# Performance work log

Hardware: AMD Instinct MI355X
Metric: run time of the kernel (lower is better)

## Reference

```python
import jax, jax.numpy as jnp
import numpy as np

B, T, E, H = 1024, 200, 128, 128
N_ITEMS, N_CATS = 100000, 1000
LN_EPS = 1e-5


def _prelu(x, a):
    return jnp.where(x >= 0, x, a * x)


def _layernorm(x, g, b):
    m = x.mean(-1, keepdims=True)
    v = ((x - m) ** 2).mean(-1, keepdims=True)
    return (x - m) / jnp.sqrt(v + LN_EPS) * g + b


def setup_inputs() -> dict:
    key = jax.random.key(0)
    it = iter(jax.random.split(key, 64))
    nx = lambda: next(it)
    def lin(out_d, in_d):
        s = 1.0 / np.sqrt(in_d)
        return jax.random.uniform(nx(), (out_d, in_d), jnp.float32, -s, s)
    inp = {}
    inp['behavior_ids'] = jax.random.randint(nx(), (B, T), 0, N_ITEMS)
    inp['candidate_id'] = jax.random.randint(nx(), (B,), 0, N_ITEMS)
    inp['candidate_cat'] = jax.random.randint(nx(), (B,), 0, N_CATS)
    inp['dense_features'] = jax.random.normal(nx(), (B, 5), jnp.float32)
    inp['item_emb'] = (jax.random.normal(nx(), (N_ITEMS, E), jnp.float32) * 0.01).at[0].set(0.0)
    inp['cat_emb'] = (jax.random.normal(nx(), (N_CATS, E // 2), jnp.float32) * 0.01).at[0].set(0.0)
    # nn.GRU params (gate order r,z,n)
    inp['gru_wih'] = lin(3 * H, E)
    inp['gru_whh'] = lin(3 * H, H)
    inp['gru_bih'] = jnp.zeros((3 * H,), jnp.float32)
    inp['gru_bhh'] = jnp.zeros((3 * H,), jnp.float32)
    # auxiliary_net: Linear(H,E) -> ReLU -> Linear(E,1)
    inp['aux_w1'] = lin(E, H); inp['aux_b1'] = jnp.zeros((E,), jnp.float32)
    inp['aux_w2'] = lin(1, E); inp['aux_b2'] = jnp.zeros((1,), jnp.float32)
    # attention_mlp: Linear(3H,64) -> PReLU -> Linear(64,1)
    inp['att_w1'] = lin(64, 3 * H); inp['att_b1'] = jnp.zeros((64,), jnp.float32)
    inp['att_a'] = jnp.array(0.25, jnp.float32)
    inp['att_w2'] = lin(1, 64); inp['att_b2'] = jnp.zeros((1,), jnp.float32)
    # AUGRU gates: Linear(2H, H) each
    inp['wz'] = lin(H, 2 * H); inp['bz'] = jnp.zeros((H,), jnp.float32)
    inp['wr'] = lin(H, 2 * H); inp['br'] = jnp.zeros((H,), jnp.float32)
    inp['wh'] = lin(H, 2 * H); inp['bh'] = jnp.zeros((H,), jnp.float32)
    # dense_proj Linear(5,32)
    inp['dp_w'] = lin(32, 5); inp['dp_b'] = jnp.zeros((32,), jnp.float32)
    # MLP: 352 -> 256 -> 128 -> 64, each Linear + LayerNorm + PReLU
    dims = [H + E + E // 2 + 32, 256, 128, 64]
    for i in range(3):
        inp[f'm_w{i+1}'] = lin(dims[i + 1], dims[i])
        inp[f'm_b{i+1}'] = jnp.zeros((dims[i + 1],), jnp.float32)
        inp[f'ln_g{i+1}'] = jnp.ones((dims[i + 1],), jnp.float32)
        inp[f'ln_b{i+1}'] = jnp.zeros((dims[i + 1],), jnp.float32)
        inp[f'pa{i+1}'] = jnp.array(0.25, jnp.float32)
    # 3 task heads Linear(64,1), stacked
    inp['heads_w'] = lin(3, 64); inp['heads_b'] = jnp.zeros((3,), jnp.float32)
    return inp


def _forward_core(behavior_ids, candidate_id, candidate_cat, dense_features,
                  item_emb, cat_emb, gru_wih, gru_whh, gru_bih, gru_bhh,
                  aux_w1, aux_b1, aux_w2, aux_b2,
                  att_w1, att_b1, att_a, att_w2, att_b2,
                  wz, bz, wr, br, wh, bh, dp_w, dp_b,
                  m_w1, m_b1, ln_g1, ln_b1, pa1,
                  m_w2, m_b2, ln_g2, ln_b2, pa2,
                  m_w3, m_b3, ln_g3, ln_b3, pa3,
                  heads_w, heads_b):
    beh = item_emb[behavior_ids]            # [B,T,E]
    cand = item_emb[candidate_id]           # [B,E]
    catv = cat_emb[candidate_cat]           # [B,E//2]
    Bsz = beh.shape[0]
    Hd = gru_whh.shape[1]
    h0 = jnp.zeros((Bsz, Hd), beh.dtype)
    # --- interest extractor GRU (cuDNN GRU math, gate order r,z,n) ---
    xp = jnp.einsum('bte,ge->btg', beh, gru_wih) + gru_bih  # [B,T,3H]
    def gru_step(h, x):
        hp = h @ gru_whh.T + gru_bhh
        xr, xz, xn = jnp.split(x, 3, -1)
        hr, hz, hn = jnp.split(hp, 3, -1)
        r = jax.nn.sigmoid(xr + hr)
        z = jax.nn.sigmoid(xz + hz)
        n = jnp.tanh(xn + r * hn)
        hnew = (1 - z) * n + z * h
        return hnew, hnew
    _, hs = jax.lax.scan(gru_step, h0, jnp.swapaxes(xp, 0, 1))
    hs = jnp.swapaxes(hs, 0, 1)             # [B,T,H]
    # --- auxiliary logits ---
    aux = jax.nn.relu(hs[:, :-1] @ aux_w1.T + aux_b1) @ aux_w2.T + aux_b2  # [B,T-1,1]
    # --- attention (embed_dim == hidden_size so cand_proj == candidate_emb) ---
    ce = cand[:, None, :]
    att_in = jnp.concatenate([hs, jnp.broadcast_to(ce, hs.shape), hs * ce], -1)  # [B,T,3H]
    scores = (_prelu(att_in @ att_w1.T + att_b1, att_a) @ att_w2.T + att_b2)[..., 0]
    att = jax.nn.softmax(scores, axis=-1)   # [B,T]
    # --- AUGRU: attention-modulated update gate ---
    def augru_step(h, xs):
        x, a = xs                           # x: [B,H], a: [B]
        comb = jnp.concatenate([x, h], -1)
        z = jax.nn.sigmoid(comb @ wz.T + bz)
        r = jax.nn.sigmoid(comb @ wr.T + br)
        comb_r = jnp.concatenate([x, r * h], -1)
        ht = jnp.tanh(comb_r @ wh.T + bh)
        zp = a[:, None] * z
        return (1 - zp) * h + zp * ht, None
    hT, _ = jax.lax.scan(augru_step, h0, (jnp.swapaxes(hs, 0, 1), att.T))
    # --- fusion MLP (dropout is identity in eval) ---
    dense_out = dense_features @ dp_w.T + dp_b
    x = jnp.concatenate([hT, cand, catv, dense_out], -1)  # [B,352]
    for (w, b, g, be, a) in ((m_w1, m_b1, ln_g1, ln_b1, pa1),
                             (m_w2, m_b2, ln_g2, ln_b2, pa2),
                             (m_w3, m_b3, ln_g3, ln_b3, pa3)):
        x = _prelu(_layernorm(x @ w.T + b, g, be), a)
    preds = jax.nn.sigmoid(x @ heads_w.T + heads_b)  # [B,3] == 3 heads of [B,1]
    return preds, aux


def reference(behavior_ids, candidate_id, candidate_cat, dense_features,
              item_emb, cat_emb, gru_wih, gru_whh, gru_bih, gru_bhh,
              aux_w1, aux_b1, aux_w2, aux_b2,
              att_w1, att_b1, att_a, att_w2, att_b2,
              wz, bz, wr, br, wh, bh, dp_w, dp_b,
              m_w1, m_b1, ln_g1, ln_b1, pa1,
              m_w2, m_b2, ln_g2, ln_b2, pa2,
              m_w3, m_b3, ln_g3, ln_b3, pa3,
              heads_w, heads_b):
    return _forward_core(behavior_ids, candidate_id, candidate_cat, dense_features,
                         item_emb, cat_emb, gru_wih, gru_whh, gru_bih, gru_bhh,
                         aux_w1, aux_b1, aux_w2, aux_b2,
                         att_w1, att_b1, att_a, att_w2, att_b2,
                         wz, bz, wr, br, wh, bh, dp_w, dp_b,
                         m_w1, m_b1, ln_g1, ln_b1, pa1,
                         m_w2, m_b2, ln_g2, ln_b2, pa2,
                         m_w3, m_b3, ln_g3, ln_b3, pa3,
                         heads_w, heads_b)
```

## Files before the change

### kernel.cpp

```cpp
#include <hip/hip_runtime.h>


typedef __bf16 bf16;
typedef float f32x4 __attribute__((ext_vector_type(4)));
typedef __bf16 bf16x8 __attribute__((ext_vector_type(8)));
typedef __bf16 bf16x4 __attribute__((ext_vector_type(4)));

#define MFMA16(a, b, c) __builtin_amdgcn_mfma_f32_16x16x32_bf16((a), (b), (c), 0, 0, 0)

#define BATCH 1024
#define SEQT 200
#define F32_ONE 0x3F800000u

__device__ __forceinline__ float sigm(float x) {
  return __builtin_amdgcn_rcpf(1.0f + __expf(-x));
}
__device__ __forceinline__ float tanh_fast(float x) {
  float ax = fabsf(x);
  float t = 1.0f - 2.0f * __builtin_amdgcn_rcpf(__expf(2.0f * ax) + 1.0f);
  return copysignf(t, x);
}

__device__ __forceinline__ void bar_lgkm() {
  asm volatile("s_waitcnt lgkmcnt(0)\n\ts_barrier" ::: "memory");
// ... 34 lines not shown
}

template <typename DT>
__device__ __forceinline__ void prep_body(
    const int* __restrict__ cid, const int* __restrict__ ccat,
    const DT* __restrict__ dense, const DT* __restrict__ item_emb,
    const DT* __restrict__ cat_emb, const DT* __restrict__ dp_w,
    const DT* __restrict__ dp_b, bf16* __restrict__ candbuf, bf16* __restrict__ xf) {
  const int b = blockIdx.x;
  const int t = threadIdx.x;
  bf16 v = (bf16)ldf(item_emb, (long)cid[b] * 128 + t);
  candbuf[b * 128 + t] = v;
  xf[(long)b * 352 + 128 + t] = v;
  if (t < 64) xf[(long)b * 352 + 256 + t] = (bf16)ldf(cat_emb, (long)ccat[b] * 64 + t);
  if (t < 32) {
    float s = ldf(dp_b, t);
    for (int k = 0; k < 5; k++) s += ldf(dense, b * 5 + k) * ldf(dp_w, t * 5 + k);
    xf[(long)b * 352 + 320 + t] = (bf16)s;
  }
}
__global__ __launch_bounds__(128) void k_prep(
    const unsigned* __restrict__ disc, const int* cid, const int* ccat,
    const void* dense, const void* item_emb, const void* cat_emb,
    const void* dp_w, const void* dp_b, bf16* candbuf, bf16* xf) {
  if (*disc == F32_ONE)
    prep_body<float>(cid, ccat, (const float*)dense, (const float*)item_emb,
                     (const float*)cat_emb, (const float*)dp_w, (const float*)dp_b, candbuf, xf);
  else
    prep_body<bf16>(cid, ccat, (const bf16*)dense, (const bf16*)item_emb,
                    (const bf16*)cat_emb, (const bf16*)dp_w, (const bf16*)dp_b, candbuf, xf);
}

template <typename DT>
__device__ __forceinline__ void gru5_body(
    const int* __restrict__ ids, const bf16* __restrict__ ieb,
    const DT* __restrict__ wih, const DT* __restrict__ whh,
    const DT* __restrict__ bih, const DT* __restrict__ bhh, bf16* __restrict__ hs,
    bf16 (*hA)[16][136], bf16 (*xb)[4][16][128]) {
  const int b0 = blockIdx.x * 16;
  const int tid = threadIdx.x;
  const int w = tid >> 6, lane = tid & 63, l15 = lane & 15, quad = lane >> 4;
  const int nc = w * 16 + l15;

  for (int i = tid; i < 2 * 16 * 136; i += 512) ((bf16*)hA)[i] = (bf16)0.0f;

  bf16x8 wir[4], wiz[4], win_[4], whr[4], whz[4], whn[4];
#pragma unroll
  for (int k = 0; k < 4; k++) {
    const long off = k * 32 + quad * 8;
    wir[k] = ld8(wih, (long)nc * 128 + off);
    wiz[k] = ld8(wih, (long)(128 + nc) * 128 + off);
    win_[k] = ld8(wih, (long)(256 + nc) * 128 + off);
    whr[k] = ld8(whh, (long)nc * 128 + off);
    whz[k] = ld8(whh, (long)(128 + nc) * 128 + off);
    whn[k] = ld8(whh, (long)(256 + nc) * 128 + off);
  }
  const float br_s = ldf(bih, nc) + ldf(bhh, nc);
  const float bz_s = ldf(bih, 128 + nc) + ldf(bhh, 128 + nc);
  const float bxn_s = ldf(bih, 256 + nc);
  const float bhn_s = ldf(bhh, 256 + nc);

  const int idrow = (tid >> 4) & 15;
  const int* idbase = ids + (long)(b0 + idrow) * SEQT;
  const int srcoff = ((tid & 15) ^ (idrow & 7)) * 8;

  auto DMA = [&](const int4 id4, int buf) {
#pragma unroll
    for (int j = 0; j < 2; j++) {
      const int slot = j * 2 + (tid >> 8);
      dma16(ieb + (long)((&id4.x)[slot]) * 128 + srcoff,
            (char*)&xb[buf][0][0][0] + (j * 512 + tid) * 16);
    }
  };

  const int srow = tid >> 5, sch = (tid & 31) * 4;
  bf16* hsb = hs + ((long)(b0 + srow) * SEQT) * 128 + sch;

  float hreg[4] = {0.f, 0.f, 0.f, 0.f};
  const f32x4 z4 = {0.f, 0.f, 0.f, 0.f};

  int4 idv = *(const int4*)(idbase);
  DMA(idv, 0);
  idv = *(const int4*)(idbase + 4);
  asm volatile("s_waitcnt vmcnt(1)" ::: "memory");
  __builtin_amdgcn_sched_barrier(0);
  __builtin_amdgcn_s_barrier();

#define GRU_STEP(P, S, WAITC)                                                  \
  {                                                                            \
    const int tt = t0 + (S);                                                   \
    bf16x8 af[4], xaf[4];                                                      \
    _Pragma("unroll") for (int k = 0; k < 4; k++) {                            \
      af[k] = *(const bf16x8*)&hA[P][l15][k * 32 + quad * 8];                  \
      xaf[k] = *(const bf16x8*)((const char*)&xb[buf][S][0][0] + l15 * 256 +   \
                                ((((k << 2) + quad) ^ (l15 & 7)) << 4));       \
    }                                                                          \
    { const int slot = tt ? tt - 1 : 0;                                        \
      bf16x4 hv = *(const bf16x4*)&hA[P][srow][sch];                           \
      *(bf16x4*)(hsb + (long)slot * 128) = hv; }                               \
    f32x4 ar = z4, az = z4, axn = z4, ahn = z4;                                \
    _Pragma("unroll") for (int k = 0; k < 4; k++) {                            \
      ar = MFMA16(xaf[k], wir[k], ar);                                         \
      az = MFMA16(xaf[k], wiz[k], az);                                         \
      axn = MFMA16(xaf[k], win_[k], axn);                                      \
    }                                                                          \
    _Pragma("unroll") for (int k = 0; k < 4; k++) {                            \
      ar = MFMA16(af[k], whr[k], ar);                                          \
      az = MFMA16(af[k], whz[k], az);                                          \
      ahn = MFMA16(af[k], whn[k], ahn);                                        \
    }                                                                          \
    _Pragma("unroll") for (int r = 0; r < 4; r++) {                            \
      float r_ = sigm(ar[r] + br_s);                                           \
      float z_ = sigm(az[r] + bz_s);                                           \
      float n_ = tanh_fast(axn[r] + bxn_s + r_ * (ahn[r] + bhn_s));            \
      float hnew = (1.0f - z_) * n_ + z_ * hreg[r];                            \
      hreg[r] = hnew;                                                          \
      hA[(P) ^ 1][quad * 4 + r][nc] = (bf16)hnew;                              \
    }                                                                          \
    if (WAITC) {                                                               \
       \
      asm volatile("s_waitcnt vmcnt(5) lgkmcnt(0)\n\ts_barrier" ::: "memory"); \
    } else {                                                                   \
      bar_lgkm();                                                              \
    }                                                                          \
  }

  for (int c = 0; c < 50; c++) {
    const int t0 = c * 4;
    const int buf = c & 1;
    if (c < 49) {
      DMA(idv, buf ^ 1);
      int nid = (c + 2) * 4; if (nid > 196) nid = 196;
      idv = *(const int4*)(idbase + nid);
    }
    GRU_STEP(0, 0, 0) GRU_STEP(1, 1, 0) GRU_STEP(0, 2, 0) GRU_STEP(1, 3, (c < 49))
  }
#undef GRU_STEP
  { bf16x4 hv = *(const bf16x4*)&hA[0][srow][sch];
    *(bf16x4*)(hsb + (long)(SEQT - 1) * 128) = hv; }
}
__global__ __launch_bounds__(512, 1) void k_gru5(
    const unsigned* __restrict__ disc, const int* ids, const bf16* ieb,
    const void* wih, const void* whh, const void* bih, const void* bhh, bf16* hs) {
  __shared__ __align__(16) bf16 hA[2][16][136];
  __shared__ __align__(16) bf16 xb[2][4][16][128];
  if (*disc == F32_ONE)
    gru5_body<float>(ids, ieb, (const float*)wih, (const float*)whh,
                     (const float*)bih, (const float*)bhh, hs, hA, xb);
  else
    gru5_body<bf16>(ids, ieb, (const bf16*)wih, (const bf16*)whh,
                    (const bf16*)bih, (const bf16*)bhh, hs, hA, xb);
}

template <typename DT>
__device__ __forceinline__ void attaux_body(
    const bf16* __restrict__ hs, const int* __restrict__ cid,
    const DT* __restrict__ item_emb,
    const DT* __restrict__ aw1, const DT* __restrict__ ab1,
    const DT* __restrict__ aw2, const DT* __restrict__ ab2,
    const DT* __restrict__ tw1, const DT* __restrict__ tb1, const DT* __restrict__ ta,
    const DT* __restrict__ tw2, const DT* __restrict__ tb2,
    float* __restrict__ sc, float* __restrict__ outaux,
    bf16 (*As)[64][128], float (*scPt)[64], float (*scPa)[64]) {
  const int t0 = blockIdx.x * 64;
  const int b0 = blockIdx.y * 16;
  const int tid = threadIdx.x, w = tid >> 6, lane = tid & 63, l15 = lane & 15, quad = lane >> 4;

  const int tn = w * 16 + l15;
  bf16x8 wth[4], wtc[4], wthc[4], wa0[4], wa1[4];
#pragma unroll
  for (int k = 0; k < 4; k++) {
    const long off = k * 32 + quad * 8;
    wth[k]  = ld8(tw1, (long)tn * 384 + off);
    wtc[k]  = ld8(tw1, (long)tn * 384 + 128 + off);
    wthc[k] = ld8(tw1, (long)tn * 384 + 256 + off);
    wa0[k]  = ld8(aw1, (long)((2 * w) * 16 + l15) * 128 + off);
    wa1[k]  = ld8(aw1, (long)((2 * w + 1) * 16 + l15) * 128 + off);
  }
  const float tb1c = ldf(tb1, tn), tw2c = ldf(tw2, tn);
  const float ab1c0 = ldf(ab1, (2 * w) * 16 + l15), aw2c0 = ldf(aw2, (2 * w) * 16 + l15);
  const float ab1c1 = ldf(ab1, (2 * w + 1) * 16 + l15), aw2c1 = ldf(aw2, (2 * w + 1) * 16 + l15);
  const float aP = ldf(ta, 0), tb2s = ldf(tb2, 0), ab2s = ldf(ab2, 0);

// ... 95 lines not shown
    const void* aw1, const void* ab1, const void* aw2, const void* ab2,
    const void* tw1, const void* tb1, const void* ta, const void* tw2, const void* tb2,
    float* sc, float* outaux) {
  __shared__ __align__(16) bf16 As[2][64][128];
  __shared__ __align__(16) float scPt[4][64];
  __shared__ __align__(16) float scPa[4][64];
  if (*disc == F32_ONE)
    attaux_body<float>(hs, cid, (const float*)item_emb,
                       (const float*)aw1, (const float*)ab1, (const float*)aw2, (const float*)ab2,
                       (const float*)tw1, (const float*)tb1, (const float*)ta,
                       (const float*)tw2, (const float*)tb2, sc, outaux, As, scPt, scPa);
  else
    attaux_body<bf16>(hs, cid, (const bf16*)item_emb,
                      (const bf16*)aw1, (const bf16*)ab1, (const bf16*)aw2, (const bf16*)ab2,
                      (const bf16*)tw1, (const bf16*)tb1, (const bf16*)ta,
                      (const bf16*)tw2, (const bf16*)tb2, sc, outaux, As, scPt, scPa);
}

__global__ __launch_bounds__(256) void k_softmax(float* __restrict__ sc) {
  const int b = blockIdx.x, tid = threadIdx.x;
  __shared__ float red[256];
  float v = (tid < SEQT) ? sc[(long)b * SEQT + tid] : -1e30f;
  red[tid] = v; __syncthreads();
  for (int s = 128; s > 0; s >>= 1) { if (tid < s) red[tid] = fmaxf(red[tid], red[tid + s]); __syncthreads(); }
  float mx = red[0]; __syncthreads();
  float e = (tid < SEQT) ? __expf(v - mx) : 0.f;
  red[tid] = e; __syncthreads();
  for (int s = 128; s > 0; s >>= 1) { if (tid < s) red[tid] += red[tid + s]; __syncthreads(); }
  float inv = 1.0f / red[0];
  if (tid < SEQT) sc[(long)b * SEQT + tid] = e * inv;
}

template <typename DT>
__device__ __forceinline__ void augru5_body(
    const bf16* __restrict__ hsrc, const float* __restrict__ att,
    const DT* __restrict__ wz, const DT* __restrict__ wr, const DT* __restrict__ wh,
    const DT* __restrict__ bzv, const DT* __restrict__ brv, const DT* __restrict__ bhv,
    bf16* __restrict__ xf_out,
    bf16 (*hA)[16][136], bf16 (*rhA)[136], float (*attL)[201],
    bf16 (*xb)[4][16][128]) {
  const int b0 = blockIdx.x * 16;
  const int tid = threadIdx.x;
  const int w = tid >> 6, lane = tid & 63, l15 = lane & 15, quad = lane >> 4;
  const int nc = w * 16 + l15;

  for (int i = tid; i < 2 * 16 * 136; i += 512) ((bf16*)hA)[i] = (bf16)0.0f;
  for (int i = tid; i < 16 * SEQT; i += 512) {
    int r = i / SEQT, c = i - r * SEQT;
    attL[r][c] = att[(long)(b0 + r) * SEQT + c];
  }

  bf16x8 wzx[4], wzh[4], wrx[4], wrh[4], whx[4], whh_[4];
#pragma unroll
  for (int k = 0; k < 4; k++) {
    const long off = k * 32 + quad * 8;
    wzx[k] = ld8(wz, (long)nc * 256 + off);
    wzh[k] = ld8(wz, (long)nc * 256 + 128 + off);
    wrx[k] = ld8(wr, (long)nc * 256 + off);
    wrh[k] = ld8(wr, (long)nc * 256 + 128 + off);
    whx[k] = ld8(wh, (long)nc * 256 + off);
    whh_[k] = ld8(wh, (long)nc * 256 + 128 + off);
  }
  const float bz_s = ldf(bzv, nc);
  const float br_s = ldf(brv, nc);
  const float bh_s = ldf(bhv, nc);

  const int drow = (tid >> 4) & 15;
  const int srcoff = ((tid & 15) ^ (drow & 7)) * 8;
  auto DMA = [&](int t0, int buf) {
#pragma unroll
    for (int j = 0; j < 2; j++) {
      const int slot = j * 2 + (tid >> 8);
      dma16(hsrc + ((long)(b0 + drow) * SEQT + t0 + slot) * 128 + srcoff,
            (char*)&xb[buf][0][0][0] + (j * 512 + tid) * 16);
    }
  };

  float hreg[4] = {0.f, 0.f, 0.f, 0.f};
  const f32x4 z4 = {0.f, 0.f, 0.f, 0.f};

  DMA(0, 0);
  asm volatile("s_waitcnt vmcnt(0)" ::: "memory");
  __builtin_amdgcn_sched_barrier(0);
  __builtin_amdgcn_s_barrier();

#define AUGRU_STEP(P, S, WAITC)                                                \
  {                                                                            \
    const int tt = t0 + (S);                                                   \
    bf16x8 af[4], xaf[4];                                                      \
    _Pragma("unroll") for (int k = 0; k < 4; k++) {                            \
      af[k] = *(const bf16x8*)&hA[P][l15][k * 32 + quad * 8];                  \
      xaf[k] = *(const bf16x8*)((const char*)&xb[buf][S][0][0] + l15 * 256 +   \
                                ((((k << 2) + quad) ^ (l15 & 7)) << 4));       \
    }                                                                          \
    f32x4 az = z4, ar = z4, axh = z4;                                          \
    _Pragma("unroll") for (int k = 0; k < 4; k++) {                            \
      az = MFMA16(xaf[k], wzx[k], az);                                         \
      ar = MFMA16(xaf[k], wrx[k], ar);                                         \
      axh = MFMA16(xaf[k], whx[k], axh);                                       \
    }                                                                          \
    _Pragma("unroll") for (int k = 0; k < 4; k++) {                            \
      az = MFMA16(af[k], wzh[k], az);                                          \
      ar = MFMA16(af[k], wrh[k], ar);                                          \
    }                                                                          \
    float zp[4];                                                               \
    _Pragma("unroll") for (int r = 0; r < 4; r++) {                            \
      float a_ = attL[quad * 4 + r][tt];                                       \
      float z_ = sigm(az[r] + bz_s);                                           \
      float r_ = sigm(ar[r] + br_s);                                           \
      zp[r] = a_ * z_;                                                         \
      rhA[quad * 4 + r][nc] = (bf16)(r_ * hreg[r]);                            \
    }                                                                          \
    bar_lgkm();                                                                \
    bf16x8 rf[4];                                                              \
    _Pragma("unroll") for (int k = 0; k < 4; k++)                              \
      rf[k] = *(const bf16x8*)&rhA[l15][k * 32 + quad * 8];                    \
    f32x4 ahh = axh;                                                           \
    _Pragma("unroll") for (int k = 0; k < 4; k++)                              \
      ahh = MFMA16(rf[k], whh_[k], ahh);                                       \
    _Pragma("unroll") for (int r = 0; r < 4; r++) {                            \
      float ht = tanh_fast(ahh[r] + bh_s);                                     \
      float hnew = (1.f - zp[r]) * hreg[r] + zp[r] * ht;                       \
      hreg[r] = hnew;                                                          \
      hA[(P) ^ 1][quad * 4 + r][nc] = (bf16)hnew;                              \
    }                                                                          \
    if (WAITC) {                                                               \
                     \
      asm volatile("s_waitcnt vmcnt(0) lgkmcnt(0)\n\ts_barrier" ::: "memory"); \
    } else {                                                                   \
      bar_lgkm();                                                              \
    }                                                                          \
  }

  for (int c = 0; c < 50; c++) {
    const int t0 = c * 4;
    const int buf = c & 1;
    if (c < 49) DMA((c + 1) * 4, buf ^ 1);
    AUGRU_STEP(0, 0, 0) AUGRU_STEP(1, 1, 0) AUGRU_STEP(0, 2, 0) AUGRU_STEP(1, 3, (c < 49))
  }
#undef AUGRU_STEP
#pragma unroll
  for (int r = 0; r < 4; r++)
    xf_out[(long)(b0 + quad * 4 + r) * 352 + nc] = (bf16)hreg[r];
}
__global__ __launch_bounds__(512, 1) void k_augru5(
    const unsigned* __restrict__ disc, const bf16* hsrc, const float* att,
    const void* wz, const void* wr, const void* wh,
    const void* bzv, const void* brv, const void* bhv, bf16* xf_out) {
  __shared__ __align__(16) bf16 hA[2][16][136];
  __shared__ __align__(16) bf16 rhA[16][136];
  __shared__ __align__(16) float attL[16][201];
  __shared__ __align__(16) bf16 xb[2][4][16][128];
  if (*disc == F32_ONE)
    augru5_body<float>(hsrc, att, (const float*)wz, (const float*)wr, (const float*)wh,
                       (const float*)bzv, (const float*)brv, (const float*)bhv, xf_out,
                       hA, rhA, attL, xb);
  else
    augru5_body<bf16>(hsrc, att, (const bf16*)wz, (const bf16*)wr, (const bf16*)wh,
                      (const bf16*)bzv, (const bf16*)brv, (const bf16*)bhv, xf_out,
                      hA, rhA, attL, xb);
}

template <typename DT>
__device__ __forceinline__ void mlp_body(
    const bf16* __restrict__ xf,
    const DT* __restrict__ w1, const DT* __restrict__ b1, const DT* __restrict__ g1, const DT* __restrict__ be1, const DT* __restrict__ pa1,
    const DT* __restrict__ w2, const DT* __restrict__ b2, const DT* __restrict__ g2, const DT* __restrict__ be2, const DT* __restrict__ pa2,
    const DT* __restrict__ w3, const DT* __restrict__ b3, const DT* __restrict__ g3, const DT* __restrict__ be3, const DT* __restrict__ pa3,
    const DT* __restrict__ hw, const DT* __restrict__ hb, float* __restrict__ preds,
    float (*xs)[352], float (*ys)[256]) {
  const int tid = threadIdx.x, w = tid >> 6, lane = tid & 63;
  const int b = blockIdx.x * 4 + w;
  for (int i = lane; i < 352; i += 64) xs[w][i] = (float)xf[(long)b * 352 + i];
  __syncthreads();
  float acc1[4];
#pragma unroll
  for (int oi = 0; oi < 4; oi++) {
    int o = lane + 64 * oi;
    float s = ldf(b1, o);
    for (int k = 0; k < 352; k += 8) {
      bf16x8 wv = ld8(w1, (long)o * 352 + k);
#pragma unroll
      for (int j = 0; j < 8; j++) s += xs[w][k + j] * (float)wv[j];
    }
    acc1[oi] = s;
  }
  float sm = acc1[0] + acc1[1] + acc1[2] + acc1[3];
#pragma unroll
  for (int m = 1; m < 64; m <<= 1) sm += __shfl_xor(sm, m, 64);
  float mean = sm * (1.0f / 256.0f);
  float vs = 0.f;
// ... 121 lines not shown
  const void* dp_b = d_in[26];
  const void* m_w1 = d_in[27];
  const void* m_b1 = d_in[28];
  const void* ln_g1 = d_in[29];
  const void* ln_b1 = d_in[30];
  const void* pa1 = d_in[31];
  const void* m_w2 = d_in[32];
  const void* m_b2 = d_in[33];
  const void* ln_g2 = d_in[34];
  const void* ln_b2 = d_in[35];
  const void* pa2 = d_in[36];
  const void* m_w3 = d_in[37];
  const void* m_b3 = d_in[38];
  const void* ln_g3 = d_in[39];
  const void* ln_b3 = d_in[40];
  const void* pa3 = d_in[41];
  const void* heads_w = d_in[42];
  const void* heads_b = d_in[43];
  (void)in_sizes; (void)n_in; (void)out_size; (void)ws_size;

  const unsigned* disc = (const unsigned*)ln_g1;

  char* ws = (char*)d_ws;
  bf16* HS = (bf16*)(ws);
  float* SC = (float*)(ws + 52428800L);
  bf16* CAND = (bf16*)(ws + 53248000L);
  bf16* XF = (bf16*)(ws + 53510144L);
  bf16* IEB = (bf16*)(ws + 54231040L);
  float* OUT = (float*)d_out;

  k_cast<<<6250, 256, 0, stream>>>(disc, item_emb, IEB);
  k_prep<<<BATCH, 128, 0, stream>>>(disc, candidate_id, candidate_cat, dense, item_emb,
                                    cat_emb, dp_w, dp_b, CAND, XF);
  k_gru5<<<64, 512, 0, stream>>>(disc, behavior_ids, IEB, gru_wih, gru_whh,
                                 gru_bih, gru_bhh, HS);
  k_attaux<<<dim3(4, 64), 256, 0, stream>>>(disc, HS, candidate_id, item_emb,
                                            aux_w1, aux_b1, aux_w2, aux_b2,
                                            att_w1, att_b1, att_a, att_w2, att_b2,
                                            SC, OUT + 3072);
  k_softmax<<<BATCH, 256, 0, stream>>>(SC);
  k_augru5<<<64, 512, 0, stream>>>(disc, HS, SC, wz, wr, wh, bz, br, bh, XF);
  k_mlp<<<256, 256, 0, stream>>>(disc, XF,
      m_w1, m_b1, ln_g1, ln_b1, pa1,
      m_w2, m_b2, ln_g2, ln_b2, pa2,
      m_w3, m_b3, ln_g3, ln_b3, pa3,
      heads_w, heads_b, OUT);
}
```

Before: 733.9 us.

## Halve GRU/AUGRU block to 4 waves, each computing two 16-column tiles

Both recurrent kernels now launch 256 threads (4 waves) per block instead of 512, and each wave handles 32 hidden columns as two 16-wide MFMA tiles. Weight fragments are doubled per wave, the DMA and hidden-state store loops are widened to cover the same data with fewer threads. The aim is cheaper per-step barriers and more independent MFMAs per wave to hide latency in the sequential loop. In exchange, register pressure roughly doubles and each wave does twice the serial gate math per step.

```diff
diff --git a/kernel.cpp b/kernel.cpp
--- a/kernel.cpp
+++ b/kernel.cpp
@@ -90,7 +90,7 @@
 }
 
 template <typename DT>
-__device__ __forceinline__ void gru5_body(
+__device__ __forceinline__ void gru6_body(
     const int* __restrict__ ids, const bf16* __restrict__ ieb,
     const DT* __restrict__ wih, const DT* __restrict__ whh,
     const DT* __restrict__ bih, const DT* __restrict__ bhh, bf16* __restrict__ hs,
@@ -98,43 +98,45 @@
   const int b0 = blockIdx.x * 16;
   const int tid = threadIdx.x;
   const int w = tid >> 6, lane = tid & 63, l15 = lane & 15, quad = lane >> 4;
-  const int nc = w * 16 + l15;
-
-  for (int i = tid; i < 2 * 16 * 136; i += 512) ((bf16*)hA)[i] = (bf16)0.0f;
-
-  bf16x8 wir[4], wiz[4], win_[4], whr[4], whz[4], whn[4];
-#pragma unroll
-  for (int k = 0; k < 4; k++) {
-    const long off = k * 32 + quad * 8;
-    wir[k] = ld8(wih, (long)nc * 128 + off);
-    wiz[k] = ld8(wih, (long)(128 + nc) * 128 + off);
-    win_[k] = ld8(wih, (long)(256 + nc) * 128 + off);
-    whr[k] = ld8(whh, (long)nc * 128 + off);
-    whz[k] = ld8(whh, (long)(128 + nc) * 128 + off);
-    whn[k] = ld8(whh, (long)(256 + nc) * 128 + off);
-  }
-  const float br_s = ldf(bih, nc) + ldf(bhh, nc);
-  const float bz_s = ldf(bih, 128 + nc) + ldf(bhh, 128 + nc);
-  const float bxn_s = ldf(bih, 256 + nc);
-  const float bhn_s = ldf(bhh, 256 + nc);
-
-  const int idrow = (tid >> 4) & 15;
-  const int* idbase = ids + (long)(b0 + idrow) * SEQT;
-  const int srcoff = ((tid & 15) ^ (idrow & 7)) * 8;
+
+  for (int i = tid; i < 2 * 16 * 136; i += 256) ((bf16*)hA)[i] = (bf16)0.0f;
+
+  bf16x8 wir[2][4], wiz[2][4], win_[2][4], whr[2][4], whz[2][4], whn[2][4];
+  float br_s[2], bz_s[2], bxn_s[2], bhn_s[2];
+#pragma unroll
+  for (int nt = 0; nt < 2; nt++) {
+    const int nc = w * 32 + nt * 16 + l15;
+#pragma unroll
+    for (int k = 0; k < 4; k++) {
+      const long off = k * 32 + quad * 8;
+      wir[nt][k] = ld8(wih, (long)nc * 128 + off);
+      wiz[nt][k] = ld8(wih, (long)(128 + nc) * 128 + off);
+      win_[nt][k] = ld8(wih, (long)(256 + nc) * 128 + off);
+      whr[nt][k] = ld8(whh, (long)nc * 128 + off);
+      whz[nt][k] = ld8(whh, (long)(128 + nc) * 128 + off);
+      whn[nt][k] = ld8(whh, (long)(256 + nc) * 128 + off);
+    }
+    br_s[nt] = ldf(bih, nc) + ldf(bhh, nc);
+    bz_s[nt] = ldf(bih, 128 + nc) + ldf(bhh, 128 + nc);
+    bxn_s[nt] = ldf(bih, 256 + nc);
+    bhn_s[nt] = ldf(bhh, 256 + nc);
+  }
+
+  const int drow = tid >> 4;
+  const int* idbase = ids + (long)(b0 + drow) * SEQT;
+  const int srcoff = ((tid & 15) ^ (drow & 7)) * 8;
 
   auto DMA = [&](const int4 id4, int buf) {
 #pragma unroll
-    for (int j = 0; j < 2; j++) {
-      const int slot = j * 2 + (tid >> 8);
-      dma16(ieb + (long)((&id4.x)[slot]) * 128 + srcoff,
-            (char*)&xb[buf][0][0][0] + (j * 512 + tid) * 16);
-    }
+    for (int j = 0; j < 4; j++)
+      dma16(ieb + (long)((&id4.x)[j]) * 128 + srcoff,
+            (char*)&xb[buf][0][0][0] + (j * 256 + tid) * 16);
   };
 
-  const int srow = tid >> 5, sch = (tid & 31) * 4;
+  const int srow = tid >> 4, sch = (tid & 15) * 8;
   bf16* hsb = hs + ((long)(b0 + srow) * SEQT) * 128 + sch;
 
-  float hreg[4] = {0.f, 0.f, 0.f, 0.f};
+  float hreg[2][4] = {{0.f, 0.f, 0.f, 0.f}, {0.f, 0.f, 0.f, 0.f}};
   const f32x4 z4 = {0.f, 0.f, 0.f, 0.f};
 
   int4 idv = *(const int4*)(idbase);
@@ -154,26 +156,33 @@
                                 ((((k << 2) + quad) ^ (l15 & 7)) << 4));       \
     }                                                                          \
     { const int slot = tt ? tt - 1 : 0;                                        \
-      bf16x4 hv = *(const bf16x4*)&hA[P][srow][sch];                           \
-      *(bf16x4*)(hsb + (long)slot * 128) = hv; }                               \
-    f32x4 ar = z4, az = z4, axn = z4, ahn = z4;                                \
-    _Pragma("unroll") for (int k = 0; k < 4; k++) {                            \
-      ar = MFMA16(xaf[k], wir[k], ar);                                         \
-      az = MFMA16(xaf[k], wiz[k], az);                                         \
-      axn = MFMA16(xaf[k], win_[k], axn);                                      \
-    }                                                                          \
-    _Pragma("unroll") for (int k = 0; k < 4; k++) {                            \
-      ar = MFMA16(af[k], whr[k], ar);                                          \
-      az = MFMA16(af[k], whz[k], az);                                          \
-      ahn = MFMA16(af[k], whn[k], ahn);                                        \
-    }                                                                          \
-    _Pragma("unroll") for (int r = 0; r < 4; r++) {                            \
-      float r_ = sigm(ar[r] + br_s);                                           \
-      float z_ = sigm(az[r] + bz_s);                                           \
-      float n_ = tanh_fast(axn[r] + bxn_s + r_ * (ahn[r] + bhn_s));            \
-      float hnew = (1.0f - z_) * n_ + z_ * hreg[r];                            \
-      hreg[r] = hnew;                                                          \
-      hA[(P) ^ 1][quad * 4 + r][nc] = (bf16)hnew;                              \
+      bf16x8 hv = *(const bf16x8*)&hA[P][srow][sch];                           \
+      *(bf16x8*)(hsb + (long)slot * 128) = hv; }                               \
+    f32x4 ar[2] = {z4, z4}, az[2] = {z4, z4}, axn[2] = {z4, z4},               \
+          ahn[2] = {z4, z4};                                                   \
+    _Pragma("unroll") for (int k = 0; k < 4; k++)                              \
+    _Pragma("unroll") for (int nt = 0; nt < 2; nt++) {                         \
+      ar[nt] = MFMA16(xaf[k], wir[nt][k], ar[nt]);                             \
+      az[nt] = MFMA16(xaf[k], wiz[nt][k], az[nt]);                             \
+      axn[nt] = MFMA16(xaf[k], win_[nt][k], axn[nt]);                          \
+    }                                                                          \
+    _Pragma("unroll") for (int k = 0; k < 4; k++)                              \
+    _Pragma("unroll") for (int nt = 0; nt < 2; nt++) {                         \
+      ar[nt] = MFMA16(af[k], whr[nt][k], ar[nt]);                              \
+      az[nt] = MFMA16(af[k], whz[nt][k], az[nt]);                              \
+      ahn[nt] = MFMA16(af[k], whn[nt][k], ahn[nt]);                            \
+    }                                                                          \
+    _Pragma("unroll") for (int nt = 0; nt < 2; nt++) {                         \
+      const int nc = w * 32 + nt * 16 + l15;                                   \
+      _Pragma("unroll") for (int r = 0; r < 4; r++) {                          \
+        float r_ = sigm(ar[nt][r] + br_s[nt]);                                 \
+        float z_ = sigm(az[nt][r] + bz_s[nt]);                                 \
+        float n_ = tanh_fast(axn[nt][r] + bxn_s[nt] +                          \
+                             r_ * (ahn[nt][r] + bhn_s[nt]));                   \
+        float hnew = (1.0f - z_) * n_ + z_ * hreg[nt][r];                      \
+        hreg[nt][r] = hnew;                                                    \
+        hA[(P) ^ 1][quad * 4 + r][nc] = (bf16)hnew;                            \
+      }                                                                        \
     }                                                                          \
     if (WAITC) {                                                               \
        \
@@ -194,19 +203,19 @@
     GRU_STEP(0, 0, 0) GRU_STEP(1, 1, 0) GRU_STEP(0, 2, 0) GRU_STEP(1, 3, (c < 49))
   }
 #undef GRU_STEP
-  { bf16x4 hv = *(const bf16x4*)&hA[0][srow][sch];
-    *(bf16x4*)(hsb + (long)(SEQT - 1) * 128) = hv; }
-}
-__global__ __launch_bounds__(512, 1) void k_gru5(
+  { bf16x8 hv = *(const bf16x8*)&hA[0][srow][sch];
+    *(bf16x8*)(hsb + (long)(SEQT - 1) * 128) = hv; }
+}
+__global__ __launch_bounds__(256, 1) void k_gru6(
     const unsigned* __restrict__ disc, const int* ids, const bf16* ieb,
     const void* wih, const void* whh, const void* bih, const void* bhh, bf16* hs) {
   __shared__ __align__(16) bf16 hA[2][16][136];
   __shared__ __align__(16) bf16 xb[2][4][16][128];
   if (*disc == F32_ONE)
-    gru5_body<float>(ids, ieb, (const float*)wih, (const float*)whh,
+    gru6_body<float>(ids, ieb, (const float*)wih, (const float*)whh,
                      (const float*)bih, (const float*)bhh, hs, hA, xb);
   else
-    gru5_body<bf16>(ids, ieb, (const bf16*)wih, (const bf16*)whh,
+    gru6_body<bf16>(ids, ieb, (const bf16*)wih, (const bf16*)whh,
                     (const bf16*)bih, (const bf16*)bhh, hs, hA, xb);
 }
 
@@ -368,7 +377,7 @@
 }
 
 template <typename DT>
-__device__ __forceinline__ void augru5_body(
+__device__ __forceinline__ void augru6_body(
     const bf16* __restrict__ hsrc, const float* __restrict__ att,
     const DT* __restrict__ wz, const DT* __restrict__ wr, const DT* __restrict__ wh,
     const DT* __restrict__ bzv, const DT* __restrict__ brv, const DT* __restrict__ bhv,
@@ -378,41 +387,43 @@
   const int b0 = blockIdx.x * 16;
   const int tid = threadIdx.x;
   const int w = tid >> 6, lane = tid & 63, l15 = lane & 15, quad = lane >> 4;
-  const int nc = w * 16 + l15;
-
-  for (int i = tid; i < 2 * 16 * 136; i += 512) ((bf16*)hA)[i] = (bf16)0.0f;
-  for (int i = tid; i < 16 * SEQT; i += 512) {
+
+  for (int i = tid; i < 2 * 16 * 136; i += 256) ((bf16*)hA)[i] = (bf16)0.0f;
+  for (int i = tid; i < 16 * SEQT; i += 256) {
     int r = i / SEQT, c = i - r * SEQT;
     attL[r][c] = att[(long)(b0 + r) * SEQT + c];
   }
 
-  bf16x8 wzx[4], wzh[4], wrx[4], wrh[4], whx[4], whh_[4];
-#pragma unroll
-  for (int k = 0; k < 4; k++) {
-    const long off = k * 32 + quad * 8;
-    wzx[k] = ld8(wz, (long)nc * 256 + off);
-    wzh[k] = ld8(wz, (long)nc * 256 + 128 + off);
-    wrx[k] = ld8(wr, (long)nc * 256 + off);
-    wrh[k] = ld8(wr, (long)nc * 256 + 128 + off);
-    whx[k] = ld8(wh, (long)nc * 256 + off);
-    whh_[k] = ld8(wh, (long)nc * 256 + 128 + off);
-  }
-  const float bz_s = ldf(bzv, nc);
-  const float br_s = ldf(brv, nc);
-  const float bh_s = ldf(bhv, nc);
-
-  const int drow = (tid >> 4) & 15;
+  bf16x8 wzx[2][4], wzh[2][4], wrx[2][4], wrh[2][4], whx[2][4], whh_[2][4];
+  float bz_s[2], br_s[2], bh_s[2];
+#pragma unroll
+  for (int nt = 0; nt < 2; nt++) {
+    const int nc = w * 32 + nt * 16 + l15;
+#pragma unroll
+    for (int k = 0; k < 4; k++) {
+      const long off = k * 32 + quad * 8;
+      wzx[nt][k] = ld8(wz, (long)nc * 256 + off);
+      wzh[nt][k] = ld8(wz, (long)nc * 256 + 128 + off);
+      wrx[nt][k] = ld8(wr, (long)nc * 256 + off);
+      wrh[nt][k] = ld8(wr, (long)nc * 256 + 128 + off);
+      whx[nt][k] = ld8(wh, (long)nc * 256 + off);
+      whh_[nt][k] = ld8(wh, (long)nc * 256 + 128 + off);
+    }
+    bz_s[nt] = ldf(bzv, nc);
+    br_s[nt] = ldf(brv, nc);
+    bh_s[nt] = ldf(bhv, nc);
+  }
+
+  const int drow = tid >> 4;
   const int srcoff = ((tid & 15) ^ (drow & 7)) * 8;
   auto DMA = [&](int t0, int buf) {
 #pragma unroll
-    for (int j = 0; j < 2; j++) {
-      const int slot = j * 2 + (tid >> 8);
-      dma16(hsrc + ((long)(b0 + drow) * SEQT + t0 + slot) * 128 + srcoff,
-            (char*)&xb[buf][0][0][0] + (j * 512 + tid) * 16);
-    }
+    for (int j = 0; j < 4; j++)
+      dma16(hsrc + ((long)(b0 + drow) * SEQT + t0 + j) * 128 + srcoff,
+            (char*)&xb[buf][0][0][0] + (j * 256 + tid) * 16);
   };
 
-  float hreg[4] = {0.f, 0.f, 0.f, 0.f};
+  float hreg[2][4] = {{0.f, 0.f, 0.f, 0.f}, {0.f, 0.f, 0.f, 0.f}};
   const f32x4 z4 = {0.f, 0.f, 0.f, 0.f};
 
   DMA(0, 0);
@@ -429,36 +440,45 @@
       xaf[k] = *(const bf16x8*)((const char*)&xb[buf][S][0][0] + l15 * 256 +   \
                                 ((((k << 2) + quad) ^ (l15 & 7)) << 4));       \
     }                                                                          \
-    f32x4 az = z4, ar = z4, axh = z4;                                          \
-    _Pragma("unroll") for (int k = 0; k < 4; k++) {                            \
-      az = MFMA16(xaf[k], wzx[k], az);                                         \
-      ar = MFMA16(xaf[k], wrx[k], ar);                                         \
-      axh = MFMA16(xaf[k], whx[k], axh);                                       \
-    }                                                                          \
-    _Pragma("unroll") for (int k = 0; k < 4; k++) {                            \
-      az = MFMA16(af[k], wzh[k], az);                                          \
-      ar = MFMA16(af[k], wrh[k], ar);                                          \
-    }                                                                          \
-    float zp[4];                                                               \
-    _Pragma("unroll") for (int r = 0; r < 4; r++) {                            \
-      float a_ = attL[quad * 4 + r][tt];                                       \
-      float z_ = sigm(az[r] + bz_s);                                           \
-      float r_ = sigm(ar[r] + br_s);                                           \
-      zp[r] = a_ * z_;                                                         \
-      rhA[quad * 4 + r][nc] = (bf16)(r_ * hreg[r]);                            \
+    f32x4 az[2] = {z4, z4}, ar[2] = {z4, z4}, axh[2] = {z4, z4};               \
+    _Pragma("unroll") for (int k = 0; k < 4; k++)                              \
+    _Pragma("unroll") for (int nt = 0; nt < 2; nt++) {                         \
+      az[nt] = MFMA16(xaf[k], wzx[nt][k], az[nt]);                             \
+      ar[nt] = MFMA16(xaf[k], wrx[nt][k], ar[nt]);                             \
+      axh[nt] = MFMA16(xaf[k], whx[nt][k], axh[nt]);                           \
+    }                                                                          \
+    _Pragma("unroll") for (int k = 0; k < 4; k++)                              \
+    _Pragma("unroll") for (int nt = 0; nt < 2; nt++) {                         \
+      az[nt] = MFMA16(af[k], wzh[nt][k], az[nt]);                              \
+      ar[nt] = MFMA16(af[k], wrh[nt][k], ar[nt]);                              \
+    }                                                                          \
+    float zp[2][4];                                                            \
+    _Pragma("unroll") for (int nt = 0; nt < 2; nt++) {                         \
+      const int nc = w * 32 + nt * 16 + l15;                                   \
+      _Pragma("unroll") for (int r = 0; r < 4; r++) {                          \
+        float a_ = attL[quad * 4 + r][tt];                                     \
+        float z_ = sigm(az[nt][r] + bz_s[nt]);                                 \
+        float r_ = sigm(ar[nt][r] + br_s[nt]);                                 \
+        zp[nt][r] = a_ * z_;                                                   \
+        rhA[quad * 4 + r][nc] = (bf16)(r_ * hreg[nt][r]);                      \
+      }                                                                        \
     }                                                                          \
     bar_lgkm();                                                                \
     bf16x8 rf[4];                                                              \
     _Pragma("unroll") for (int k = 0; k < 4; k++)                              \
       rf[k] = *(const bf16x8*)&rhA[l15][k * 32 + quad * 8];                    \
-    f32x4 ahh = axh;                                                           \
+    f32x4 ahh[2] = {axh[0], axh[1]};                                           \
     _Pragma("unroll") for (int k = 0; k < 4; k++)                              \
-      ahh = MFMA16(rf[k], whh_[k], ahh);                                       \
-    _Pragma("unroll") for (int r = 0; r < 4; r++) {                            \
-      float ht = tanh_fast(ahh[r] + bh_s);                                     \
-      float hnew = (1.f - zp[r]) * hreg[r] + zp[r] * ht;                       \
-      hreg[r] = hnew;                                                          \
-      hA[(P) ^ 1][quad * 4 + r][nc] = (bf16)hnew;                              \
+    _Pragma("unroll") for (int nt = 0; nt < 2; nt++)                           \
+      ahh[nt] = MFMA16(rf[k], whh_[nt][k], ahh[nt]);                           \
+    _Pragma("unroll") for (int nt = 0; nt < 2; nt++) {                         \
+      const int nc = w * 32 + nt * 16 + l15;                                   \
+      _Pragma("unroll") for (int r = 0; r < 4; r++) {                          \
+        float ht = tanh_fast(ahh[nt][r] + bh_s[nt]);                           \
+        float hnew = (1.f - zp[nt][r]) * hreg[nt][r] + zp[nt][r] * ht;         \
+        hreg[nt][r] = hnew;                                                    \
+        hA[(P) ^ 1][quad * 4 + r][nc] = (bf16)hnew;                            \
+      }                                                                        \
     }                                                                          \
     if (WAITC) {                                                               \
                      \
@@ -476,10 +496,14 @@
   }
 #undef AUGRU_STEP
 #pragma unroll
-  for (int r = 0; r < 4; r++)
-    xf_out[(long)(b0 + quad * 4 + r) * 352 + nc] = (bf16)hreg[r];
-}
-__global__ __launch_bounds__(512, 1) void k_augru5(
+  for (int nt = 0; nt < 2; nt++) {
+    const int nc = w * 32 + nt * 16 + l15;
+#pragma unroll
+    for (int r = 0; r < 4; r++)
+      xf_out[(long)(b0 + quad * 4 + r) * 352 + nc] = (bf16)hreg[nt][r];
+  }
+}
+__global__ __launch_bounds__(256, 1) void k_augru6(
     const unsigned* __restrict__ disc, const bf16* hsrc, const float* att,
     const void* wz, const void* wr, const void* wh,
     const void* bzv, const void* brv, const void* bhv, bf16* xf_out) {
@@ -488,11 +512,11 @@
   __shared__ __align__(16) float attL[16][201];
   __shared__ __align__(16) bf16 xb[2][4][16][128];
   if (*disc == F32_ONE)
-    augru5_body<float>(hsrc, att, (const float*)wz, (const float*)wr, (const float*)wh,
+    augru6_body<float>(hsrc, att, (const float*)wz, (const float*)wr, (const float*)wh,
                        (const float*)bzv, (const float*)brv, (const float*)bhv, xf_out,
                        hA, rhA, attL, xb);
   else
-    augru5_body<bf16>(hsrc, att, (const bf16*)wz, (const bf16*)wr, (const bf16*)wh,
+    augru6_body<bf16>(hsrc, att, (const bf16*)wz, (const bf16*)wr, (const bf16*)wh,
                       (const bf16*)bzv, (const bf16*)brv, (const bf16*)bhv, xf_out,
                       hA, rhA, attL, xb);
 }
@@ -680,14 +704,14 @@
   k_cast<<<6250, 256, 0, stream>>>(disc, item_emb, IEB);
   k_prep<<<BATCH, 128, 0, stream>>>(disc, candidate_id, candidate_cat, dense, item_emb,
                                     cat_emb, dp_w, dp_b, CAND, XF);
-  k_gru5<<<64, 512, 0, stream>>>(disc, behavior_ids, IEB, gru_wih, gru_whh,
+  k_gru6<<<64, 256, 0, stream>>>(disc, behavior_ids, IEB, gru_wih, gru_whh,
                                  gru_bih, gru_bhh, HS);
   k_attaux<<<dim3(4, 64), 256, 0, stream>>>(disc, HS, candidate_id, item_emb,
                                             aux_w1, aux_b1, aux_w2, aux_b2,
                                             att_w1, att_b1, att_a, att_w2, att_b2,
                                             SC, OUT + 3072);
   k_softmax<<<BATCH, 256, 0, stream>>>(SC);
-  k_augru5<<<64, 512, 0, stream>>>(disc, HS, SC, wz, wr, wh, bz, br, bh, XF);
+  k_augru6<<<64, 256, 0, stream>>>(disc, HS, SC, wz, wr, wh, bz, br, bh, XF);
   k_mlp<<<256, 256, 0, stream>>>(disc, XF,
       m_w1, m_b1, ln_g1, ln_b1, pa1,
       m_w2, m_b2, ln_g2, ln_b2, pa2,
```

Result: slower. 818.6 us (+11.5%).

## Pack two batch groups per 1024-thread block in GRU and AUGRU kernels

Applied to the files above, without the earlier changes.

The GRU and AUGRU recurrence kernels now launch 32 blocks of 1024 threads instead of 64 blocks of 512. Each block runs two independent 16-row batch groups, each with its own shared-memory state, buffers and attention slice, and both groups share the per-step barriers. The aim is to interleave two independent recurrence chains on one CU so that each chain's latency is hidden behind the other. In exchange, half as many CUs are in use and each SIMD carries twice the waves and MFMA work. The 1024-thread launch bound also caps registers per thread, which risks spilling the roughly 96 registers of weight fragments held per wave.

```diff
diff --git a/kernel.cpp b/kernel.cpp
--- a/kernel.cpp
+++ b/kernel.cpp
@@ -90,17 +90,18 @@
 }
 
 template <typename DT>
-__device__ __forceinline__ void gru5_body(
+__device__ __forceinline__ void gru7_body(
     const int* __restrict__ ids, const bf16* __restrict__ ieb,
     const DT* __restrict__ wih, const DT* __restrict__ whh,
     const DT* __restrict__ bih, const DT* __restrict__ bhh, bf16* __restrict__ hs,
-    bf16 (*hA)[16][136], bf16 (*xb)[4][16][128]) {
-  const int b0 = blockIdx.x * 16;
+    bf16 (*hA)[2][16][136], bf16 (*xb)[2][4][16][128]) {
   const int tid = threadIdx.x;
-  const int w = tid >> 6, lane = tid & 63, l15 = lane & 15, quad = lane >> 4;
+  const int p = tid >> 9, t5 = tid & 511;
+  const int b0 = blockIdx.x * 32 + p * 16;
+  const int w = t5 >> 6, lane = tid & 63, l15 = lane & 15, quad = lane >> 4;
   const int nc = w * 16 + l15;
 
-  for (int i = tid; i < 2 * 16 * 136; i += 512) ((bf16*)hA)[i] = (bf16)0.0f;
+  for (int i = tid; i < 2 * 2 * 16 * 136; i += 1024) ((bf16*)hA)[i] = (bf16)0.0f;
 
   bf16x8 wir[4], wiz[4], win_[4], whr[4], whz[4], whn[4];
 #pragma unroll
@@ -118,20 +119,20 @@
   const float bxn_s = ldf(bih, 256 + nc);
   const float bhn_s = ldf(bhh, 256 + nc);
 
-  const int idrow = (tid >> 4) & 15;
-  const int* idbase = ids + (long)(b0 + idrow) * SEQT;
-  const int srcoff = ((tid & 15) ^ (idrow & 7)) * 8;
+  const int drow = (t5 >> 4) & 15;
+  const int* idbase = ids + (long)(b0 + drow) * SEQT;
+  const int srcoff = ((t5 & 15) ^ (drow & 7)) * 8;
 
   auto DMA = [&](const int4 id4, int buf) {
 #pragma unroll
     for (int j = 0; j < 2; j++) {
-      const int slot = j * 2 + (tid >> 8);
+      const int slot = j * 2 + (t5 >> 8);
       dma16(ieb + (long)((&id4.x)[slot]) * 128 + srcoff,
-            (char*)&xb[buf][0][0][0] + (j * 512 + tid) * 16);
+            (char*)&xb[p][buf][0][0][0] + (j * 512 + t5) * 16);
     }
   };
 
-  const int srow = tid >> 5, sch = (tid & 31) * 4;
+  const int srow = t5 >> 5, sch = (t5 & 31) * 4;
   bf16* hsb = hs + ((long)(b0 + srow) * SEQT) * 128 + sch;
 
   float hreg[4] = {0.f, 0.f, 0.f, 0.f};
@@ -149,12 +150,13 @@
     const int tt = t0 + (S);                                                   \
     bf16x8 af[4], xaf[4];                                                      \
     _Pragma("unroll") for (int k = 0; k < 4; k++) {                            \
-      af[k] = *(const bf16x8*)&hA[P][l15][k * 32 + quad * 8];                  \
-      xaf[k] = *(const bf16x8*)((const char*)&xb[buf][S][0][0] + l15 * 256 +   \
+      af[k] = *(const bf16x8*)&hA[p][P][l15][k * 32 + quad * 8];               \
+      xaf[k] = *(const bf16x8*)((const char*)&xb[p][buf][S][0][0] +            \
+                                l15 * 256 +                                    \
                                 ((((k << 2) + quad) ^ (l15 & 7)) << 4));       \
     }                                                                          \
     { const int slot = tt ? tt - 1 : 0;                                        \
-      bf16x4 hv = *(const bf16x4*)&hA[P][srow][sch];                           \
+      bf16x4 hv = *(const bf16x4*)&hA[p][P][srow][sch];                        \
       *(bf16x4*)(hsb + (long)slot * 128) = hv; }                               \
     f32x4 ar = z4, az = z4, axn = z4, ahn = z4;                                \
     _Pragma("unroll") for (int k = 0; k < 4; k++) {                            \
@@ -173,7 +175,7 @@
       float n_ = tanh_fast(axn[r] + bxn_s + r_ * (ahn[r] + bhn_s));            \
       float hnew = (1.0f - z_) * n_ + z_ * hreg[r];                            \
       hreg[r] = hnew;                                                          \
-      hA[(P) ^ 1][quad * 4 + r][nc] = (bf16)hnew;                              \
+      hA[p][(P) ^ 1][quad * 4 + r][nc] = (bf16)hnew;                           \
     }                                                                          \
     if (WAITC) {                                                               \
        \
@@ -194,19 +196,19 @@
     GRU_STEP(0, 0, 0) GRU_STEP(1, 1, 0) GRU_STEP(0, 2, 0) GRU_STEP(1, 3, (c < 49))
   }
 #undef GRU_STEP
-  { bf16x4 hv = *(const bf16x4*)&hA[0][srow][sch];
+  { bf16x4 hv = *(const bf16x4*)&hA[p][0][srow][sch];
     *(bf16x4*)(hsb + (long)(SEQT - 1) * 128) = hv; }
 }
-__global__ __launch_bounds__(512, 1) void k_gru5(
+__global__ __launch_bounds__(1024, 1) void k_gru7(
     const unsigned* __restrict__ disc, const int* ids, const bf16* ieb,
     const void* wih, const void* whh, const void* bih, const void* bhh, bf16* hs) {
-  __shared__ __align__(16) bf16 hA[2][16][136];
-  __shared__ __align__(16) bf16 xb[2][4][16][128];
+  __shared__ __align__(16) bf16 hA[2][2][16][136];
+  __shared__ __align__(16) bf16 xb[2][2][4][16][128];
   if (*disc == F32_ONE)
-    gru5_body<float>(ids, ieb, (const float*)wih, (const float*)whh,
+    gru7_body<float>(ids, ieb, (const float*)wih, (const float*)whh,
                      (const float*)bih, (const float*)bhh, hs, hA, xb);
   else
-    gru5_body<bf16>(ids, ieb, (const bf16*)wih, (const bf16*)whh,
+    gru7_body<bf16>(ids, ieb, (const bf16*)wih, (const bf16*)whh,
                     (const bf16*)bih, (const bf16*)bhh, hs, hA, xb);
 }
 
@@ -368,22 +370,25 @@
 }
 
 template <typename DT>
-__device__ __forceinline__ void augru5_body(
+__device__ __forceinline__ void augru7_body(
     const bf16* __restrict__ hsrc, const float* __restrict__ att,
     const DT* __restrict__ wz, const DT* __restrict__ wr, const DT* __restrict__ wh,
     const DT* __restrict__ bzv, const DT* __restrict__ brv, const DT* __restrict__ bhv,
     bf16* __restrict__ xf_out,
-    bf16 (*hA)[16][136], bf16 (*rhA)[136], float (*attL)[201],
-    bf16 (*xb)[4][16][128]) {
-  const int b0 = blockIdx.x * 16;
+    bf16 (*hA)[2][16][136], bf16 (*rhA)[16][136], float (*attL)[16][201],
+    bf16 (*xb)[2][4][16][128]) {
   const int tid = threadIdx.x;
-  const int w = tid >> 6, lane = tid & 63, l15 = lane & 15, quad = lane >> 4;
+  const int p = tid >> 9, t5 = tid & 511;
+  const int b0 = blockIdx.x * 32 + p * 16;
+  const int w = t5 >> 6, lane = tid & 63, l15 = lane & 15, quad = lane >> 4;
   const int nc = w * 16 + l15;
 
-  for (int i = tid; i < 2 * 16 * 136; i += 512) ((bf16*)hA)[i] = (bf16)0.0f;
-  for (int i = tid; i < 16 * SEQT; i += 512) {
-    int r = i / SEQT, c = i - r * SEQT;
-    attL[r][c] = att[(long)(b0 + r) * SEQT + c];
+  for (int i = tid; i < 2 * 2 * 16 * 136; i += 1024) ((bf16*)hA)[i] = (bf16)0.0f;
+  for (int i = tid; i < 2 * 16 * SEQT; i += 1024) {
+    int pp = i / (16 * SEQT);
+    int rem = i - pp * 16 * SEQT;
+    int r = rem / SEQT, c = rem - r * SEQT;
+    attL[pp][r][c] = att[(long)(blockIdx.x * 32 + pp * 16 + r) * SEQT + c];
   }
 
   bf16x8 wzx[4], wzh[4], wrx[4], wrh[4], whx[4], whh_[4];
@@ -401,14 +406,14 @@
   const float br_s = ldf(brv, nc);
   const float bh_s = ldf(bhv, nc);
 
-  const int drow = (tid >> 4) & 15;
-  const int srcoff = ((tid & 15) ^ (drow & 7)) * 8;
+  const int drow = (t5 >> 4) & 15;
+  const int srcoff = ((t5 & 15) ^ (drow & 7)) * 8;
   auto DMA = [&](int t0, int buf) {
 #pragma unroll
     for (int j = 0; j < 2; j++) {
-      const int slot = j * 2 + (tid >> 8);
+      const int slot = j * 2 + (t5 >> 8);
       dma16(hsrc + ((long)(b0 + drow) * SEQT + t0 + slot) * 128 + srcoff,
-            (char*)&xb[buf][0][0][0] + (j * 512 + tid) * 16);
+            (char*)&xb[p][buf][0][0][0] + (j * 512 + t5) * 16);
     }
   };
 
@@ -425,8 +430,9 @@
     const int tt = t0 + (S);                                                   \
     bf16x8 af[4], xaf[4];                                                      \
     _Pragma("unroll") for (int k = 0; k < 4; k++) {                            \
-      af[k] = *(const bf16x8*)&hA[P][l15][k * 32 + quad * 8];                  \
-      xaf[k] = *(const bf16x8*)((const char*)&xb[buf][S][0][0] + l15 * 256 +   \
+      af[k] = *(const bf16x8*)&hA[p][P][l15][k * 32 + quad * 8];               \
+      xaf[k] = *(const bf16x8*)((const char*)&xb[p][buf][S][0][0] +            \
+                                l15 * 256 +                                    \
                                 ((((k << 2) + quad) ^ (l15 & 7)) << 4));       \
     }                                                                          \
     f32x4 az = z4, ar = z4, axh = z4;                                          \
@@ -441,16 +447,16 @@
     }                                                                          \
     float zp[4];                                                               \
     _Pragma("unroll") for (int r = 0; r < 4; r++) {                            \
-      float a_ = attL[quad * 4 + r][tt];                                       \
+      float a_ = attL[p][quad * 4 + r][tt];                                    \
       float z_ = sigm(az[r] + bz_s);                                           \
       float r_ = sigm(ar[r] + br_s);                                           \
       zp[r] = a_ * z_;                                                         \
-      rhA[quad * 4 + r][nc] = (bf16)(r_ * hreg[r]);                            \
+      rhA[p][quad * 4 + r][nc] = (bf16)(r_ * hreg[r]);                         \
     }                                                                          \
     bar_lgkm();                                                                \
     bf16x8 rf[4];                                                              \
     _Pragma("unroll") for (int k = 0; k < 4; k++)                              \
-      rf[k] = *(const bf16x8*)&rhA[l15][k * 32 + quad * 8];                    \
+      rf[k] = *(const bf16x8*)&rhA[p][l15][k * 32 + quad * 8];                 \
     f32x4 ahh = axh;                                                           \
     _Pragma("unroll") for (int k = 0; k < 4; k++)                              \
       ahh = MFMA16(rf[k], whh_[k], ahh);                                       \
@@ -458,7 +464,7 @@
       float ht = tanh_fast(ahh[r] + bh_s);                                     \
       float hnew = (1.f - zp[r]) * hreg[r] + zp[r] * ht;                       \
       hreg[r] = hnew;                                                          \
-      hA[(P) ^ 1][quad * 4 + r][nc] = (bf16)hnew;                              \
+      hA[p][(P) ^ 1][quad * 4 + r][nc] = (bf16)hnew;                           \
     }                                                                          \
     if (WAITC) {                                                               \
                      \
@@ -479,20 +485,20 @@
   for (int r = 0; r < 4; r++)
     xf_out[(long)(b0 + quad * 4 + r) * 352 + nc] = (bf16)hreg[r];
 }
-__global__ __launch_bounds__(512, 1) void k_augru5(
+__global__ __launch_bounds__(1024, 1) void k_augru7(
     const unsigned* __restrict__ disc, const bf16* hsrc, const float* att,
     const void* wz, const void* wr, const void* wh,
     const void* bzv, const void* brv, const void* bhv, bf16* xf_out) {
-  __shared__ __align__(16) bf16 hA[2][16][136];
-  __shared__ __align__(16) bf16 rhA[16][136];
-  __shared__ __align__(16) float attL[16][201];
-  __shared__ __align__(16) bf16 xb[2][4][16][128];
+  __shared__ __align__(16) bf16 hA[2][2][16][136];
+  __shared__ __align__(16) bf16 rhA[2][16][136];
+  __shared__ __align__(16) float attL[2][16][201];
+  __shared__ __align__(16) bf16 xb[2][2][4][16][128];
   if (*disc == F32_ONE)
-    augru5_body<float>(hsrc, att, (const float*)wz, (const float*)wr, (const float*)wh,
+    augru7_body<float>(hsrc, att, (const float*)wz, (const float*)wr, (const float*)wh,
                        (const float*)bzv, (const float*)brv, (const float*)bhv, xf_out,
                        hA, rhA, attL, xb);
   else
-    augru5_body<bf16>(hsrc, att, (const bf16*)wz, (const bf16*)wr, (const bf16*)wh,
+    augru7_body<bf16>(hsrc, att, (const bf16*)wz, (const bf16*)wr, (const bf16*)wh,
                       (const bf16*)bzv, (const bf16*)brv, (const bf16*)bhv, xf_out,
                       hA, rhA, attL, xb);
 }
@@ -680,14 +686,14 @@
   k_cast<<<6250, 256, 0, stream>>>(disc, item_emb, IEB);
   k_prep<<<BATCH, 128, 0, stream>>>(disc, candidate_id, candidate_cat, dense, item_emb,
                                     cat_emb, dp_w, dp_b, CAND, XF);
-  k_gru5<<<64, 512, 0, stream>>>(disc, behavior_ids, IEB, gru_wih, gru_whh,
-                                 gru_bih, gru_bhh, HS);
+  k_gru7<<<32, 1024, 0, stream>>>(disc, behavior_ids, IEB, gru_wih, gru_whh,
+                                  gru_bih, gru_bhh, HS);
   k_attaux<<<dim3(4, 64), 256, 0, stream>>>(disc, HS, candidate_id, item_emb,
                                             aux_w1, aux_b1, aux_w2, aux_b2,
                                             att_w1, att_b1, att_a, att_w2, att_b2,
                                             SC, OUT + 3072);
   k_softmax<<<BATCH, 256, 0, stream>>>(SC);
-  k_augru5<<<64, 512, 0, stream>>>(disc, HS, SC, wz, wr, wh, bz, br, bh, XF);
+  k_augru7<<<32, 1024, 0, stream>>>(disc, HS, SC, wz, wr, wh, bz, br, bh, XF);
   k_mlp<<<256, 256, 0, stream>>>(disc, XF,
       m_w1, m_b1, ln_g1, ln_b1, pa1,
       m_w2, m_b2, ln_g2, ln_b2, pa2,
```

Measured after the change: 2.128 ms. +190.0%, slower.
